# Optimization experiments

Measured on AMD Instinct MI355X. Metric: run time of the kernel, lower is better.

Reference implementation:

```python
import jax, jax.numpy as jnp
import numpy as np

B, N, D_IN = 4, 2048, 768
D_OUT, H = 768, 12
HD = D_OUT // H  # 64


def setup_inputs() -> dict:
    key = jax.random.key(0)
    ks = jax.random.split(key, 6)
    s = 0.02
    return {
        "x": jax.random.normal(ks[0], (B, N, D_IN), dtype=jnp.float32),
        "W_q": jax.random.normal(ks[1], (D_IN, D_OUT), dtype=jnp.float32) * s,
        "W_k": jax.random.normal(ks[2], (D_IN, D_OUT), dtype=jnp.float32) * s,
        "W_v": jax.random.normal(ks[3], (D_IN, D_OUT), dtype=jnp.float32) * s,
        "W_o": jax.random.normal(ks[4], (D_OUT, D_OUT), dtype=jnp.float32) * s,
        "b_o": jax.random.normal(ks[5], (D_OUT,), dtype=jnp.float32) * s,
    }


def reference(x, W_q, W_k, W_v, W_o, b_o):
    b, n, _ = x.shape
    # project and split heads: [b, h, n, hd]
    q = (x @ W_q).reshape(b, n, H, HD).transpose(0, 2, 1, 3)
    k = (x @ W_k).reshape(b, n, H, HD).transpose(0, 2, 1, 3)
    v = (x @ W_v).reshape(b, n, H, HD).transpose(0, 2, 1, 3)
    scores = jnp.einsum("bhqd,bhkd->bhqk", q, k)
    causal = jnp.tril(jnp.ones((n, n), dtype=bool))
    scores = jnp.where(causal, scores, -jnp.inf)
    w = jax.nn.softmax(scores / jnp.sqrt(jnp.float32(HD)), axis=-1)
    ctx = jnp.einsum("bhqk,bhkd->bhqd", w, v)
    ctx = ctx.transpose(0, 2, 1, 3).reshape(b, n, D_OUT)
    return ctx @ W_o + b_o
```

## Files before the change

kernel.cpp:

```cpp
#include <hip/hip_runtime.h>
#include <hip/hip_bf16.h>
#include <stdint.h>

typedef unsigned short u16;
typedef __attribute__((ext_vector_type(8))) short short8;
typedef __attribute__((ext_vector_type(4))) float f32x4;
typedef __attribute__((ext_vector_type(16))) float f32x16;

#define GLOBAL_AS __attribute__((address_space(1)))
#define LDS_AS __attribute__((address_space(3)))

#define BB 4
#define NSEQ 2048
#define DIN 768
#define DOUT 768
#define NH 12
#define HD 64
#define MROWS (BB*NSEQ)

static __device__ __forceinline__ u16 f2bf(float f) {
  union { float f; uint32_t u; } v; v.f = f;
  uint32_t r = (v.u + 0x7fffu + ((v.u >> 16) & 1u)) >> 16;
  return (u16)r;
}
static __device__ __forceinline__ uint32_t pack2b(float lo, float hi) {
  union { __hip_bfloat162 h; uint32_t u; } cv;
  cv.h.x = __float2bfloat16(lo);
  cv.h.y = __float2bfloat16(hi);
  return cv.u;
}

__global__ __launch_bounds__(256) void convert2_k(const float* __restrict__ x,
                          const float* __restrict__ Wq, const float* __restrict__ Wk,
                          const float* __restrict__ Wv, const float* __restrict__ Wo,
                          u16* __restrict__ xb, u16* __restrict__ WqT,
                          u16* __restrict__ WkT, u16* __restrict__ WvT,
                          u16* __restrict__ WoT) {
  int tid = threadIdx.x;
  if (blockIdx.x < 576) {
    int wi = blockIdx.x;
    int which = wi / 144, t = wi % 144;
    int tr = t / 12, tc = t % 12;
    const float* src = which==0 ? Wq : which==1 ? Wk : which==2 ? Wv : Wo;
    u16* dst = which==0 ? WqT : which==1 ? WkT : which==2 ? WvT : WoT;
    __shared__ u16 lt[64][65];
    int r0 = tid >> 6, c = tid & 63;
#pragma unroll
    for (int rr=0; rr<16; rr++) {
      int row = rr*4 + r0;
      lt[row][c] = f2bf(src[(size_t)(tr*64+row)*DOUT + tc*64 + c]);
    }
    __syncthreads();
#pragma unroll
    for (int rr=0; rr<16; rr++) {
      int row = rr*4 + r0;
      dst[(size_t)(tc*64+row)*DIN + tr*64 + c] = lt[c][row];
    }
  } else {
    const float4* x4 = (const float4*)x;
    uint2* o4 = (uint2*)xb;
    int n4 = MROWS*DIN/4;
    int i = (int)(blockIdx.x - 576) * 256 + tid;
    for (; i < n4; i += 2048*256) {
      float4 v = x4[i];
      uint2 o; o.x = pack2b(v.x, v.y); o.y = pack2b(v.z, v.w);
      o4[i] = o;
    }
  }
}

__global__ __launch_bounds__(256) void gemm_qkv_k(const u16* __restrict__ A,
                                                  const u16* __restrict__ Bt,
                                                  u16* __restrict__ Qg,
                                                  u16* __restrict__ Kgo,
                                                  u16* __restrict__ Vto) {
  const int K = DIN;
  int xcd = blockIdx.x & 7, j = blockIdx.x >> 3;
  int m0 = (xcd*8 + (j & 7)) * 128;
  int nt = j >> 3;
  nt = (nt % 3) * 6 + nt / 3;
  int n0 = nt * 128;
  int tid = threadIdx.x;
  int lane = tid & 63, wid = tid >> 6;
  int wr = wid >> 1, wc = wid & 1;
  int g = lane >> 4, r = lane & 15;

  __shared__ __attribute__((aligned(16))) u16 sbuf[128*129];
  u16* lA = sbuf;
  u16* lB = sbuf + 8192;

  auto stage = [&](int buf, int k0) {
#pragma unroll
    for (int i=0;i<2;i++) {
      int ch = wid*2 + i;
      int e = ch*512 + lane*8;
      int row = e >> 5, col = e & 31;
      __builtin_amdgcn_global_load_lds(
        (GLOBAL_AS void*)(A + (size_t)(m0+row)*K + k0 + col),
        (LDS_AS void*)(&lA[buf*4096 + ch*512]), 16, 0, 0);
      __builtin_amdgcn_global_load_lds(
        (GLOBAL_AS void*)(Bt + (size_t)(n0+row)*K + k0 + col),
        (LDS_AS void*)(&lB[buf*4096 + ch*512]), 16, 0, 0);
    }
  };

  f32x4 acc[4][4];
#pragma unroll
  for (int i=0;i<4;i++)
#pragma unroll
    for (int jj=0;jj<4;jj++) acc[i][jj] = (f32x4){0.f,0.f,0.f,0.f};

  stage(0, 0);
  int buf = 0;
  for (int k0 = 0; k0 < K; k0 += 32) {
    asm volatile("s_waitcnt vmcnt(0)" ::: "memory");
    __builtin_amdgcn_s_barrier();
    asm volatile("" ::: "memory");
    if (k0 + 32 < K) stage(buf ^ 1, k0 + 32);

    short8 af[4], bf[4];
#pragma unroll
    for (int f=0; f<4; f++) {
      af[f] = *(const short8*)&lA[buf*4096 + (wr*64 + f*16 + r)*32 + g*8];
      bf[f] = *(const short8*)&lB[buf*4096 + (wc*64 + f*16 + r)*32 + g*8];
    }
#pragma unroll
    for (int fr=0; fr<4; fr++)
#pragma unroll
      for (int fc=0; fc<4; fc++)
        acc[fr][fc] = __builtin_amdgcn_mfma_f32_16x16x32_bf16(af[fr], bf[fc], acc[fr][fc], 0, 0, 0);
    buf ^= 1;
  }
  __syncthreads();

  if (n0 < 1536) {
    bool isQ = n0 < 768;
    u16* outb = isQ ? Qg : Kgo;
    int nb = isQ ? n0 : n0 - 768;
#pragma unroll
    for (int fr=0; fr<4; fr++)
#pragma unroll
      for (int fc=0; fc<4; fc++)
#pragma unroll
        for (int v=0; v<4; v++) {
          int row = m0 + wr*64 + fr*16 + g*4 + v;
          int cc  = nb + wc*64 + fc*16 + r;
          int b = row >> 11, nn = row & (NSEQ-1);
          float val = acc[fr][fc][v];
          if (isQ) val *= 0.18033688f;
          outb[(((size_t)b*NH + (cc>>6))*NSEQ + nn)*HD + (cc&63)] = f2bf(val);
        }
  } else {
    int nb = n0 - 1536;
#pragma unroll
    for (int fr=0; fr<4; fr++)
#pragma unroll
      for (int fc=0; fc<4; fc++)
#pragma unroll
        for (int v=0; v<4; v++) {
          int ii = wr*64 + fr*16 + g*4 + v;
          int jj = wc*64 + fc*16 + r;
          sbuf[ii*129 + jj] = f2bf(acc[fr][fc][v]);
        }
    __syncthreads();
    int b = m0 >> 11;
#pragma unroll 1
    for (int rep=0; rep<64; rep++) {
      int flat = rep*256 + tid;
      int jj = flat >> 7, ii = flat & 127;
      int cc = nb + jj;
      int nn = (m0 + ii) & (NSEQ-1);
      Vto[(((size_t)b*NH + (cc>>6))*HD + (cc&63))*NSEQ + nn] = sbuf[ii*129 + jj];
    }
  }
}

__global__ __launch_bounds__(256) void gemm_o_k(const u16* __restrict__ A,
                                                const u16* __restrict__ Bt,
                                                float* __restrict__ outf,
                                                const float* __restrict__ bias) {
  const int K = DIN;
  int xcd = blockIdx.x & 7, j = blockIdx.x >> 3;
  int m0 = (xcd*8 + (j & 7)) * 128;
  int n0 = (j >> 3) * 128;
  int tid = threadIdx.x;
  int lane = tid & 63, wid = tid >> 6;
  int wr = wid >> 1, wc = wid & 1;
  int g = lane >> 4, r = lane & 15;

  __shared__ __attribute__((aligned(16))) u16 lA[2][4096];
  __shared__ __attribute__((aligned(16))) u16 lB[2][4096];

  auto stage = [&](int buf, int k0) {
#pragma unroll
    for (int i=0;i<2;i++) {
      int ch = wid*2 + i;
      int e = ch*512 + lane*8;
      int row = e >> 5, col = e & 31;
      __builtin_amdgcn_global_load_lds(
        (GLOBAL_AS void*)(A + (size_t)(m0+row)*K + k0 + col),
        (LDS_AS void*)(&lA[buf][ch*512]), 16, 0, 0);
      __builtin_amdgcn_global_load_lds(
        (GLOBAL_AS void*)(Bt + (size_t)(n0+row)*K + k0 + col),
        (LDS_AS void*)(&lB[buf][ch*512]), 16, 0, 0);
    }
  };

  f32x4 acc[4][4];
#pragma unroll
  for (int i=0;i<4;i++)
#pragma unroll
    for (int jj=0;jj<4;jj++) acc[i][jj] = (f32x4){0.f,0.f,0.f,0.f};

  stage(0, 0);
  int buf = 0;
  for (int k0 = 0; k0 < K; k0 += 32) {
    asm volatile("s_waitcnt vmcnt(0)" ::: "memory");
    __builtin_amdgcn_s_barrier();
    asm volatile("" ::: "memory");
    if (k0 + 32 < K) stage(buf ^ 1, k0 + 32);

    short8 af[4], bf[4];
#pragma unroll
    for (int f=0; f<4; f++) {
      af[f] = *(const short8*)&lA[buf][(wr*64 + f*16 + r)*32 + g*8];
      bf[f] = *(const short8*)&lB[buf][(wc*64 + f*16 + r)*32 + g*8];
    }
#pragma unroll
    for (int fr=0; fr<4; fr++)
#pragma unroll
      for (int fc=0; fc<4; fc++)
        acc[fr][fc] = __builtin_amdgcn_mfma_f32_16x16x32_bf16(af[fr], bf[fc], acc[fr][fc], 0, 0, 0);
    buf ^= 1;
  }

#pragma unroll
  for (int fr=0; fr<4; fr++)
#pragma unroll
    for (int fc=0; fc<4; fc++)
#pragma unroll
      for (int v=0; v<4; v++) {
        int row = m0 + wr*64 + fr*16 + g*4 + v;
        int cc  = n0 + wc*64 + fc*16 + r;
        outf[(size_t)row*DOUT + cc] = acc[fr][fc][v] + bias[cc];
      }
}

__global__ __launch_bounds__(256, 4) void attn7_k(const u16* __restrict__ Q,
                                                  const u16* __restrict__ Kg,
                                                  const u16* __restrict__ Vt,
                                                  u16* __restrict__ ctx) {
  int i = blockIdx.x;
  int xcd = i & 7, j = i >> 3;
  int bh = xcd * 6 + (j >> 5);
  int chunk = 31 - (j & 31);
  int nkt = chunk + 1;
  int lane = threadIdx.x & 63;
  int w = threadIdx.x >> 6;
  int p = w >> 1;
  int ch = w & 1;
  int col = lane & 31;
  int hi = lane >> 5;
  int sw = (col & 7) << 4;

  const u16* Qb = Q  + (size_t)bh * NSEQ * HD;
  const u16* Kb = Kg + (size_t)bh * NSEQ * HD;
  const u16* Vb = Vt + (size_t)bh * HD * NSEQ;

  __shared__ __attribute__((aligned(16))) char smem[2][16384];

  auto stage = [&](int buf, int k0) {
#pragma unroll
    for (int ii=0; ii<2; ii++) {
      int cb = (w*2+ii) * 1024;
      int d  = cb + lane*16;
      int row = d >> 7;
      int src = (d & 127) ^ ((row & 7) << 4);
      __builtin_amdgcn_global_load_lds(
        (GLOBAL_AS void*)((const char*)Kb + (size_t)(k0+row)*128 + src),
        (LDS_AS void*)(&smem[buf][cb]), 16, 0, 0);
      __builtin_amdgcn_global_load_lds(
        (GLOBAL_AS void*)((const char*)Vb + (size_t)row*(NSEQ*2) + (size_t)k0*2 + src),
        (LDS_AS void*)(&smem[buf][8192+cb]), 16, 0, 0);
    }
  };

  int qw0 = chunk*64 + p*32;
  int q = qw0 + col;

  short8 qf[4];
#pragma unroll
  for (int ksl = 0; ksl < 4; ksl++)
    qf[ksl] = *(const short8*)&Qb[(size_t)q * HD + ksl*16 + hi*8];

  short8 ones8;
#pragma unroll
  for (int z=0; z<8; z++) ones8[z] = (short)0x3F80;

  f32x16 od[2], ol;
#pragma unroll
  for (int z=0; z<16; z++) { od[0][z] = 0.f; od[1][z] = 0.f; ol[z] = 0.f; }

  stage(0, 0);

#pragma unroll 1
  for (int t = 0; t < nkt; t++) {
    asm volatile("s_waitcnt vmcnt(0)" ::: "memory");
    __builtin_amdgcn_s_barrier();
    asm volatile("" ::: "memory");

    if (t + 1 < nkt) stage((t+1) & 1, (t+1)*64);

    int k0c = t*64 + ch*32;
    if (k0c <= qw0 + 31) {
      const char* Kt = &smem[t & 1][0];
      const char* Vtile = &smem[t & 1][8192];
      f32x16 s;
#pragma unroll
      for (int z=0; z<16; z++) s[z] = 0.f;
#pragma unroll
      for (int ksl=0; ksl<4; ksl++) {
        short8 kf = *(const short8*)(Kt + (ch*32+col)*128 + ((ksl*32 + hi*16) ^ sw));
        s = __builtin_amdgcn_mfma_f32_32x32x16_bf16(kf, qf[ksl], s, 0, 0, 0);
      }
      if (k0c + 31 > qw0) {
#pragma unroll
        for (int r2=0; r2<16; r2++) {
          int kv = k0c + (r2&3) + 8*(r2>>2) + 4*hi;
          if (kv > q) s[r2] = -1e30f;
        }
      }
      uint32_t a[8];
#pragma unroll
      for (int ww=0; ww<8; ww++) {
        float p0 = __builtin_amdgcn_exp2f(s[2*ww]);
        float p1 = __builtin_amdgcn_exp2f(s[2*ww+1]);
        a[ww] = pack2b(p0, p1);
      }

      uint32_t b[8];
#pragma unroll
      for (int ww=0; ww<8; ww++) b[ww] = (uint32_t)__shfl_xor((int)a[ww], 32);
      union { uint32_t wdat[4]; short8 s8; } u0, u1;
      u0.wdat[0] = hi ? b[2]   : a[0];
      u0.wdat[1] = hi ? b[3]   : a[1];
      u0.wdat[2] = hi ? a[2]   : b[0];
      u0.wdat[3] = hi ? a[3]   : b[1];
      u1.wdat[0] = hi ? b[6]   : a[4];
      u1.wdat[1] = hi ? b[7]   : a[5];
      u1.wdat[2] = hi ? a[6]   : b[4];
      u1.wdat[3] = hi ? a[7]   : b[5];
#pragma unroll
      for (int dc=0; dc<2; dc++) {
        short8 vf0 = *(const short8*)(Vtile + (dc*32+col)*128 + ((ch*64 + hi*16) ^ sw));
        od[dc] = __builtin_amdgcn_mfma_f32_32x32x16_bf16(vf0, u0.s8, od[dc], 0, 0, 0);
        short8 vf1 = *(const short8*)(Vtile + (dc*32+col)*128 + ((ch*64 + 32 + hi*16) ^ sw));
        od[dc] = __builtin_amdgcn_mfma_f32_32x32x16_bf16(vf1, u1.s8, od[dc], 0, 0, 0);
      }
      ol = __builtin_amdgcn_mfma_f32_32x32x16_bf16(ones8, u0.s8, ol, 0, 0, 0);
      ol = __builtin_amdgcn_mfma_f32_32x32x16_bf16(ones8, u1.s8, ol, 0, 0, 0);
    }
  }
  __syncthreads();

  float* mg = (float*)&smem[0][0] + p * (33*64);
  if (ch) {
#pragma unroll
    for (int dc=0; dc<2; dc++)
#pragma unroll
      for (int jj=0; jj<16; jj++) mg[(dc*16+jj)*64 + lane] = od[dc][jj];
    mg[32*64 + lane] = ol[0];
  }
  __syncthreads();
  if (!ch) {
    float inv = 1.0f / (ol[0] + mg[32*64 + lane]);
    int b = bh / NH, h = bh % NH;
    u16* cp_ = ctx + ((size_t)b * NSEQ + q) * DOUT + h * HD;
#pragma unroll
    for (int dc=0; dc<2; dc++)
#pragma unroll
      for (int t4=0; t4<4; t4++) {
        int d0 = dc*32 + t4*8 + hi*4;
        float v0 = (od[dc][t4*4+0] + mg[(dc*16+t4*4+0)*64 + lane]) * inv;
        float v1 = (od[dc][t4*4+1] + mg[(dc*16+t4*4+1)*64 + lane]) * inv;
        float v2 = (od[dc][t4*4+2] + mg[(dc*16+t4*4+2)*64 + lane]) * inv;
        float v3 = (od[dc][t4*4+3] + mg[(dc*16+t4*4+3)*64 + lane]) * inv;
        *(uint32_t*)(cp_ + d0)     = pack2b(v0, v1);
        *(uint32_t*)(cp_ + d0 + 2) = pack2b(v2, v3);
      }
  }
}

extern "C" void kernel_launch(void* const* d_in, const int* in_sizes, int n_in,
                              void* d_out, int out_size, void* d_ws, size_t ws_size,
                              hipStream_t stream) {
  const float* x   = (const float*)d_in[0];
  const float* Wq  = (const float*)d_in[1];
  const float* Wk  = (const float*)d_in[2];
  const float* Wv  = (const float*)d_in[3];
  const float* Wo  = (const float*)d_in[4];
  const float* bo  = (const float*)d_in[5];
  float* out = (float*)d_out;

  u16* ws  = (u16*)d_ws;
  u16* xb  = ws;
  u16* WqT = xb  + (size_t)MROWS*DIN;
  u16* WkT = WqT + (size_t)DIN*DOUT;
  u16* WvT = WkT + (size_t)DIN*DOUT;
  u16* WoT = WvT + (size_t)DIN*DOUT;
  u16* Qg  = WoT + (size_t)DIN*DOUT;
  u16* Kg  = Qg  + (size_t)MROWS*DOUT;
  u16* Vt  = Kg  + (size_t)MROWS*DOUT;
  u16* ctx = Vt  + (size_t)MROWS*DOUT;

  convert2_k<<<2624, 256, 0, stream>>>(x, Wq, Wk, Wv, Wo, xb, WqT, WkT, WvT, WoT);

  gemm_qkv_k<<<1152, 256, 0, stream>>>(xb, WqT, Qg, Kg, Vt);

  attn7_k<<<1536, 256, 0, stream>>>(Qg, Kg, Vt, ctx);

  gemm_o_k<<<384, 256, 0, stream>>>(ctx, WoT, out, bo);
}
```

Baseline: 136.4 us.

## Swizzle GEMM LDS tiles, unroll k-loop by two, use permlane32 swap in attention

Both GEMM kernels now write global-to-LDS tiles with an XOR swizzle on the 16-byte column slot and read them back with the matching swizzle, to cut LDS bank conflicts on the fragment reads. The k-loop is manually unrolled by two with fixed buffer indices, which removes the runtime buffer toggle. In the attention kernel, eight cross-half shuffles plus selects are replaced with four v_permlane32_swap instructions that exchange the P fragments between the two 32-lane halves. The inline asm swap must match the previous lane mapping exactly, otherwise results are wrong.

```diff
diff --git a/kernel.cpp b/kernel.cpp
--- a/kernel.cpp
+++ b/kernel.cpp
@@ -89,18 +89,19 @@
   u16* lA = sbuf;
   u16* lB = sbuf + 8192;
 
+  int srow0 = (wid*2)*16 + (lane >> 2);
+  int sslot = (lane & 3) ^ ((lane >> 2) & 3);
   auto stage = [&](int buf, int k0) {
 #pragma unroll
     for (int i=0;i<2;i++) {
       int ch = wid*2 + i;
-      int e = ch*512 + lane*8;
-      int row = e >> 5, col = e & 31;
-      __builtin_amdgcn_global_load_lds(
-        (GLOBAL_AS void*)(A + (size_t)(m0+row)*K + k0 + col),
-        (LDS_AS void*)(&lA[buf*4096 + ch*512]), 16, 0, 0);
-      __builtin_amdgcn_global_load_lds(
-        (GLOBAL_AS void*)(Bt + (size_t)(n0+row)*K + k0 + col),
-        (LDS_AS void*)(&lB[buf*4096 + ch*512]), 16, 0, 0);
+      int row = srow0 + i*16;
+      __builtin_amdgcn_global_load_lds(
+        (GLOBAL_AS void*)(A + (size_t)(m0+row)*K + k0 + sslot*8),
+        (LDS_AS void*)(&lA[buf*4096 + ch*512 + (lane&63)*8]), 16, 0, 0);
+      __builtin_amdgcn_global_load_lds(
+        (GLOBAL_AS void*)(Bt + (size_t)(n0+row)*K + k0 + sslot*8),
+        (LDS_AS void*)(&lB[buf*4096 + ch*512 + (lane&63)*8]), 16, 0, 0);
     }
   };
 
@@ -110,26 +111,33 @@
 #pragma unroll
     for (int jj=0;jj<4;jj++) acc[i][jj] = (f32x4){0.f,0.f,0.f,0.f};
 
+  int rsw = (r & 3);
+  auto compute = [&](int buf, int k0) {
+    short8 af[4], bf[4];
+#pragma unroll
+    for (int f=0; f<4; f++) {
+      af[f] = *(const short8*)&lA[buf*4096 + (wr*64 + f*16 + r)*32 + ((g ^ rsw)*8)];
+      bf[f] = *(const short8*)&lB[buf*4096 + (wc*64 + f*16 + r)*32 + ((g ^ rsw)*8)];
+    }
+#pragma unroll
+    for (int fr=0; fr<4; fr++)
+#pragma unroll
+      for (int fc=0; fc<4; fc++)
+        acc[fr][fc] = __builtin_amdgcn_mfma_f32_16x16x32_bf16(af[fr], bf[fc], acc[fr][fc], 0, 0, 0);
+  };
+
   stage(0, 0);
-  int buf = 0;
-  for (int k0 = 0; k0 < K; k0 += 32) {
+  for (int k0 = 0; k0 < K; k0 += 64) {
     asm volatile("s_waitcnt vmcnt(0)" ::: "memory");
     __builtin_amdgcn_s_barrier();
     asm volatile("" ::: "memory");
-    if (k0 + 32 < K) stage(buf ^ 1, k0 + 32);
-
-    short8 af[4], bf[4];
-#pragma unroll
-    for (int f=0; f<4; f++) {
-      af[f] = *(const short8*)&lA[buf*4096 + (wr*64 + f*16 + r)*32 + g*8];
-      bf[f] = *(const short8*)&lB[buf*4096 + (wc*64 + f*16 + r)*32 + g*8];
-    }
-#pragma unroll
-    for (int fr=0; fr<4; fr++)
-#pragma unroll
-      for (int fc=0; fc<4; fc++)
-        acc[fr][fc] = __builtin_amdgcn_mfma_f32_16x16x32_bf16(af[fr], bf[fc], acc[fr][fc], 0, 0, 0);
-    buf ^= 1;
+    stage(1, k0 + 32);
+    compute(0, k0);
+    asm volatile("s_waitcnt vmcnt(0)" ::: "memory");
+    __builtin_amdgcn_s_barrier();
+    asm volatile("" ::: "memory");
+    if (k0 + 64 < K) stage(0, k0 + 64);
+    compute(1, k0 + 32);
   }
   __syncthreads();
 
@@ -191,18 +199,19 @@
   __shared__ __attribute__((aligned(16))) u16 lA[2][4096];
   __shared__ __attribute__((aligned(16))) u16 lB[2][4096];
 
+  int srow0 = (wid*2)*16 + (lane >> 2);
+  int sslot = (lane & 3) ^ ((lane >> 2) & 3);
   auto stage = [&](int buf, int k0) {
 #pragma unroll
     for (int i=0;i<2;i++) {
       int ch = wid*2 + i;
-      int e = ch*512 + lane*8;
-      int row = e >> 5, col = e & 31;
-      __builtin_amdgcn_global_load_lds(
-        (GLOBAL_AS void*)(A + (size_t)(m0+row)*K + k0 + col),
-        (LDS_AS void*)(&lA[buf][ch*512]), 16, 0, 0);
-      __builtin_amdgcn_global_load_lds(
-        (GLOBAL_AS void*)(Bt + (size_t)(n0+row)*K + k0 + col),
-        (LDS_AS void*)(&lB[buf][ch*512]), 16, 0, 0);
+      int row = srow0 + i*16;
+      __builtin_amdgcn_global_load_lds(
+        (GLOBAL_AS void*)(A + (size_t)(m0+row)*K + k0 + sslot*8),
+        (LDS_AS void*)(&lA[buf][ch*512 + (lane&63)*8]), 16, 0, 0);
+      __builtin_amdgcn_global_load_lds(
+        (GLOBAL_AS void*)(Bt + (size_t)(n0+row)*K + k0 + sslot*8),
+        (LDS_AS void*)(&lB[buf][ch*512 + (lane&63)*8]), 16, 0, 0);
     }
   };
 
@@ -212,26 +221,33 @@
 #pragma unroll
     for (int jj=0;jj<4;jj++) acc[i][jj] = (f32x4){0.f,0.f,0.f,0.f};
 
+  int rsw = (r & 3);
+  auto compute = [&](int buf, int k0) {
+    short8 af[4], bf[4];
+#pragma unroll
+    for (int f=0; f<4; f++) {
+      af[f] = *(const short8*)&lA[buf][(wr*64 + f*16 + r)*32 + ((g ^ rsw)*8)];
+      bf[f] = *(const short8*)&lB[buf][(wc*64 + f*16 + r)*32 + ((g ^ rsw)*8)];
+    }
+#pragma unroll
+    for (int fr=0; fr<4; fr++)
+#pragma unroll
+      for (int fc=0; fc<4; fc++)
+        acc[fr][fc] = __builtin_amdgcn_mfma_f32_16x16x32_bf16(af[fr], bf[fc], acc[fr][fc], 0, 0, 0);
+  };
+
   stage(0, 0);
-  int buf = 0;
-  for (int k0 = 0; k0 < K; k0 += 32) {
+  for (int k0 = 0; k0 < K; k0 += 64) {
     asm volatile("s_waitcnt vmcnt(0)" ::: "memory");
     __builtin_amdgcn_s_barrier();
     asm volatile("" ::: "memory");
-    if (k0 + 32 < K) stage(buf ^ 1, k0 + 32);
-
-    short8 af[4], bf[4];
-#pragma unroll
-    for (int f=0; f<4; f++) {
-      af[f] = *(const short8*)&lA[buf][(wr*64 + f*16 + r)*32 + g*8];
-      bf[f] = *(const short8*)&lB[buf][(wc*64 + f*16 + r)*32 + g*8];
-    }
-#pragma unroll
-    for (int fr=0; fr<4; fr++)
-#pragma unroll
-      for (int fc=0; fc<4; fc++)
-        acc[fr][fc] = __builtin_amdgcn_mfma_f32_16x16x32_bf16(af[fr], bf[fc], acc[fr][fc], 0, 0, 0);
-    buf ^= 1;
+    stage(1, k0 + 32);
+    compute(0, k0);
+    asm volatile("s_waitcnt vmcnt(0)" ::: "memory");
+    __builtin_amdgcn_s_barrier();
+    asm volatile("" ::: "memory");
+    if (k0 + 64 < K) stage(0, k0 + 64);
+    compute(1, k0 + 32);
   }
 
 #pragma unroll
@@ -246,7 +262,7 @@
       }
 }
 
-__global__ __launch_bounds__(256, 4) void attn7_k(const u16* __restrict__ Q,
+__global__ __launch_bounds__(256, 4) void attn8_k(const u16* __restrict__ Q,
                                                   const u16* __restrict__ Kg,
                                                   const u16* __restrict__ Vt,
                                                   u16* __restrict__ ctx) {
@@ -338,18 +354,16 @@
         a[ww] = pack2b(p0, p1);
       }
 
-      uint32_t b[8];
-#pragma unroll
-      for (int ww=0; ww<8; ww++) b[ww] = (uint32_t)__shfl_xor((int)a[ww], 32);
+      uint32_t w0=a[0], w2=a[2], w1=a[1], w3=a[3];
+      asm volatile("v_permlane32_swap_b32 %0, %1" : "+v"(w0), "+v"(w2));
+      asm volatile("v_permlane32_swap_b32 %0, %1" : "+v"(w1), "+v"(w3));
+      uint32_t w4=a[4], w6=a[6], w5=a[5], w7=a[7];
+      asm volatile("v_permlane32_swap_b32 %0, %1" : "+v"(w4), "+v"(w6));
+      asm volatile("v_permlane32_swap_b32 %0, %1" : "+v"(w5), "+v"(w7));
       union { uint32_t wdat[4]; short8 s8; } u0, u1;
-      u0.wdat[0] = hi ? b[2]   : a[0];
-      u0.wdat[1] = hi ? b[3]   : a[1];
-      u0.wdat[2] = hi ? a[2]   : b[0];
-      u0.wdat[3] = hi ? a[3]   : b[1];
-      u1.wdat[0] = hi ? b[6]   : a[4];
-      u1.wdat[1] = hi ? b[7]   : a[5];
-      u1.wdat[2] = hi ? a[6]   : b[4];
-      u1.wdat[3] = hi ? a[7]   : b[5];
+      u0.wdat[0]=w0; u0.wdat[1]=w1; u0.wdat[2]=w2; u0.wdat[3]=w3;
+      u1.wdat[0]=w4; u1.wdat[1]=w5; u1.wdat[2]=w6; u1.wdat[3]=w7;
+
 #pragma unroll
       for (int dc=0; dc<2; dc++) {
         short8 vf0 = *(const short8*)(Vtile + (dc*32+col)*128 + ((ch*64 + hi*16) ^ sw));
@@ -417,7 +431,7 @@
 
   gemm_qkv_k<<<1152, 256, 0, stream>>>(xb, WqT, Qg, Kg, Vt);
 
-  attn7_k<<<1536, 256, 0, stream>>>(Qg, Kg, Vt, ctx);
+  attn8_k<<<1536, 256, 0, stream>>>(Qg, Kg, Vt, ctx);
 
   gemm_o_k<<<384, 256, 0, stream>>>(ctx, WoT, out, bo);
 }
```

Result: faster. 132.4 us (-3.0%).
